# Performance work log

Hardware: AMD Instinct MI355X
Metric: run time of the kernel (lower is better)

Reference implementation:

```python
import jax, jax.numpy as jnp
import numpy as np

B, S, D = 2, 2048, 1024
H = 16
HD = D // H

def setup_inputs() -> dict:
    key = jax.random.key(0)
    ks = jax.random.split(key, 9)
    s = 1.0 / np.sqrt(D)
    return {
        "x": jax.random.normal(ks[0], (B, S, D), dtype=jnp.float32),
        "Wq": jax.random.normal(ks[1], (D, D), dtype=jnp.float32) * s,
        "bq": jnp.zeros((D,), dtype=jnp.float32),
        "Wk": jax.random.normal(ks[2], (D, D), dtype=jnp.float32) * s,
        "bk": jnp.zeros((D,), dtype=jnp.float32),
        "Wv": jax.random.normal(ks[3], (D, D), dtype=jnp.float32) * s,
        "bv": jnp.zeros((D,), dtype=jnp.float32),
        "Wo": jax.random.normal(ks[4], (D, D), dtype=jnp.float32) * s,
        "bo": jnp.zeros((D,), dtype=jnp.float32),
    }

def reference(x, Wq, bq, Wk, bk, Wv, bv, Wo, bo):
    b, s, d = x.shape
    # torch Linear: y = x @ W.T + b
    def proj(W, bias):
        y = jnp.einsum('bsd,ed->bse', x, W) + bias
        return y.reshape(b, s, H, HD).transpose(0, 2, 1, 3)  # [b,h,s,hd]
    Q = proj(Wq, bq)
    K = proj(Wk, bk)
    V = proj(Wv, bv)
    scale = 1.0 / jnp.sqrt(jnp.float32(HD))
    scores = jnp.einsum('bhqd,bhkd->bhqk', Q, K) * scale  # [b,h,s,s]
    attn = jax.nn.softmax(scores, axis=-1)
    out = jnp.einsum('bhqk,bhkd->bhqd', attn, V)  # [b,h,s,hd]
    out = out.transpose(0, 2, 1, 3).reshape(b, s, d)
    return jnp.einsum('bsd,ed->bse', out, Wo) + bo
```

## Files before the change

kernel.cpp:

```cpp
#include <hip/hip_runtime.h>
#include <stdint.h>


typedef __bf16 bf16x8 __attribute__((ext_vector_type(8)));
typedef float  f32x4  __attribute__((ext_vector_type(4)));
typedef unsigned short u16x8 __attribute__((ext_vector_type(8)));

#define LOG2E 1.44269504088896f
#define FIXED_MAX_BITS 14.4269504088896f

__device__ __forceinline__ unsigned short f2bf(float f) {
    union { float f; unsigned u; } v; v.f = f;
    unsigned r = v.u + 0x7FFFu + ((v.u >> 16) & 1u);
    return (unsigned short)(r >> 16);
}
__device__ __forceinline__ float bf2f(unsigned short u) {
    union { unsigned u; float f; } v; v.u = (unsigned)u << 16; return v.f;
}

__device__ __forceinline__ float exp2_fast(float x) {
#if __has_builtin(__builtin_amdgcn_exp2f)
    return __builtin_amdgcn_exp2f(x);
#else
    return __expf(x * 0.69314718056f);
#endif
}

__device__ __forceinline__ void glds16(const void* g, void* l) {
    __builtin_amdgcn_global_load_lds(
        (__attribute__((address_space(1))) void*)(g),
        (__attribute__((address_space(3))) void*)(l),
        16, 0, 0);
}

__global__ __launch_bounds__(256) void cvt_all(
    const float* __restrict__ x,  const float* __restrict__ Wq,
    const float* __restrict__ Wk, const float* __restrict__ Wv,
    const float* __restrict__ Wo,
    unsigned short* __restrict__ xb,  unsigned short* __restrict__ Wqb,
    unsigned short* __restrict__ Wkb, unsigned short* __restrict__ Wvb,
    unsigned short* __restrict__ Wob)
{
    const int stride = gridDim.x * blockDim.x;
    for (int i = blockIdx.x * blockDim.x + threadIdx.x; i < 2097152; i += stride) {
        const float* src; unsigned short* dst; int j;
        if (i < 1048576) { src = x; dst = xb; j = i; }
        else {
            int t = (i - 1048576) >> 18; j = (i - 1048576) & 262143;
            src = (t == 0) ? Wq : (t == 1) ? Wk : (t == 2) ? Wv : Wo;
            dst = (t == 0) ? Wqb : (t == 1) ? Wkb : (t == 2) ? Wvb : Wob;
        }
        float4 v = ((const float4*)src)[j];
        ushort4 o;
        o.x = f2bf(v.x); o.y = f2bf(v.y); o.z = f2bf(v.z); o.w = f2bf(v.w);
        ((ushort4*)dst)[j] = o;
    }
}

template <int MODE>
__global__ __launch_bounds__(256) void gemm_bt(
    const unsigned short* __restrict__ A,
    const unsigned short* __restrict__ W0,
    const unsigned short* __restrict__ W1,
    const unsigned short* __restrict__ W2,
    const float* __restrict__ b0,
    const float* __restrict__ b1,
    const float* __restrict__ b2,
    unsigned short* __restrict__ outQ,
    unsigned short* __restrict__ outK,
    unsigned short* __restrict__ outV,
    float* __restrict__ outF)
{
    constexpr int BM = (MODE == 0) ? 128 : 64;
    constexpr int FM = BM / 32;
    constexpr int RA = BM / 32;

    __shared__ __attribute__((aligned(16))) unsigned short As[BM * 64];
    __shared__ __attribute__((aligned(16))) unsigned short Bs[128 * 64];

    const int tid  = threadIdx.x;
    const int lane = tid & 63;
    const int wid  = tid >> 6;
    const int quad = lane >> 4;
    const int l16  = lane & 15;

    const int m0 = blockIdx.x * BM;

    const unsigned short* W;
    const float* bias;
    int proj, n0;
    if (MODE == 0) {
        proj = blockIdx.y >> 3;
        n0   = (blockIdx.y & 7) * 128;
        W    = (proj == 0) ? W0 : (proj == 1) ? W1 : W2;
        bias = (proj == 0) ? b0 : (proj == 1) ? b1 : b2;
    } else {
        proj = 0;
        n0   = blockIdx.y * 128;
        W    = W0;
        bias = b0;
    }

    const int wm = (wid >> 1) * (BM / 2);
    const int wn = (wid & 1) * 64;

    f32x4 acc[FM][4];
#pragma unroll
    for (int i = 0; i < FM; ++i)
#pragma unroll
        for (int j = 0; j < 4; ++j)
            acc[i][j] = (f32x4){0.f, 0.f, 0.f, 0.f};

    char* AsB  = (char*)As;
    char* BsB  = (char*)Bs;
    char* ldsA = AsB + wid * 1024;
    char* ldsB = BsB + wid * 1024;

    for (int k0 = 0; k0 < 1024; k0 += 64) {
#pragma unroll
        for (int q = 0; q < RA; ++q) {
            int i   = q * 256 + tid;
            int row = i >> 3;
            int sc  = (i & 7) ^ (row & 7);
            glds16(A + (size_t)(m0 + row) * 1024 + k0 + sc * 8, ldsA + q * 4096);
        }
#pragma unroll
        for (int q = 0; q < 4; ++q) {
            int i   = q * 256 + tid;
            int row = i >> 3;
            int sc  = (i & 7) ^ (row & 7);
            glds16(W + (size_t)(n0 + row) * 1024 + k0 + sc * 8, ldsB + q * 4096);
        }
        __syncthreads();

#pragma unroll
        for (int kh = 0; kh < 2; ++kh) {
            bf16x8 af[FM], bfr[4];
#pragma unroll
            for (int t = 0; t < FM; ++t) {
                int r = wm + t * 16 + l16;
                int c = (kh * 4 + quad) ^ (r & 7);
                af[t] = *(const bf16x8*)(AsB + r * 128 + c * 16);
            }
#pragma unroll
            for (int t = 0; t < 4; ++t) {
                int r = wn + t * 16 + l16;
                int c = (kh * 4 + quad) ^ (r & 7);
                bfr[t] = *(const bf16x8*)(BsB + r * 128 + c * 16);
            }
#pragma unroll
            for (int i = 0; i < FM; ++i)
#pragma unroll
                for (int j = 0; j < 4; ++j)
                    acc[i][j] = __builtin_amdgcn_mfma_f32_16x16x32_bf16(
                        af[i], bfr[j], acc[i][j], 0, 0, 0);
        }
        __syncthreads();
    }

#pragma unroll
    for (int i = 0; i < FM; ++i) {
        const int mrow0 = m0 + wm + i * 16 + quad * 4;
#pragma unroll
        for (int j = 0; j < 4; ++j) {
            const int n  = n0 + wn + j * 16 + l16;
            const float bb = bias[n];
            if (MODE == 1) {
#pragma unroll
                for (int r = 0; r < 4; ++r)
                    outF[(size_t)(mrow0 + r) * 1024 + n] = acc[i][j][r] + bb;
            } else {
                const int h = n >> 6, hd = n & 63;
                if (proj == 2) {
                    const int b = mrow0 >> 11, s = mrow0 & 2047;
                    ushort4 pk;
                    pk.x = f2bf(acc[i][j][0] + bb);
                    pk.y = f2bf(acc[i][j][1] + bb);
                    pk.z = f2bf(acc[i][j][2] + bb);
                    pk.w = f2bf(acc[i][j][3] + bb);
                    *(ushort4*)(outV + ((size_t)((b * 16 + h) * 64 + hd)) * 2048 + s) = pk;
                } else {
                    unsigned short* dst = (proj == 0) ? outQ : outK;
                    const float scl = (proj == 0) ? (0.125f * LOG2E) : 1.0f;
#pragma unroll
                    for (int r = 0; r < 4; ++r) {
                        const int m = mrow0 + r;
                        const int b = m >> 11, s = m & 2047;
                        dst[((size_t)((b * 16 + h) * 2048 + s)) * 64 + hd] =
                            f2bf((acc[i][j][r] + bb) * scl);
                    }
                }
            }
        }
    }
}

__global__ __launch_bounds__(256, 4) void attn_kernel(
    const unsigned short* __restrict__ Qb,
    const unsigned short* __restrict__ Kb,
    const unsigned short* __restrict__ Vtb,
    unsigned short* __restrict__ attnb)
{
    __shared__ __attribute__((aligned(16))) unsigned short Ks[128 * 64];
    __shared__ __attribute__((aligned(16))) unsigned short Vs[2 * 64 * 64];

    const int tid  = threadIdx.x;
    const int lane = tid & 63;
    const int wid  = tid >> 6;
    const int quad = lane >> 4;
    const int l16  = lane & 15;
    const int l7   = l16 & 7;

    const int q0   = blockIdx.x * 128 + wid * 32;
    const int hb   = blockIdx.y;
    const int bq   = hb >> 4, hh = hb & 15;

    const unsigned short* Qh  = Qb  + (size_t)hb * 2048 * 64;
    const unsigned short* Kh  = Kb  + (size_t)hb * 2048 * 64;
    const unsigned short* Vth = Vtb + (size_t)hb * 64 * 2048;

    bf16x8 qf[2][2];
#pragma unroll
    for (int qt = 0; qt < 2; ++qt) {
        const unsigned short* qp = Qh + (size_t)(q0 + qt * 16 + l16) * 64 + quad * 8;
        qf[qt][0] = *(const bf16x8*)(qp);
        qf[qt][1] = *(const bf16x8*)(qp + 32);
    }

    f32x4 o[4][2];
#pragma unroll
    for (int ht = 0; ht < 4; ++ht)
#pragma unroll
        for (int qt = 0; qt < 2; ++qt)
            o[ht][qt] = (f32x4){0.f, 0.f, 0.f, 0.f};
    float lsum[2] = {0.f, 0.f};

    char* KsB  = (char*)Ks;
    char* ldsK = KsB + wid * 1024;

    const int base_row = 8 * (l16 >> 2) + (l16 & 3);
    const int kp0 = ((quad) ^ l7) * 16;
    const int kp1 = ((4 + quad) ^ l7) * 16;
    const int vrow = l16 * 128;

    for (int kc = 0; kc < 2048; kc += 128) {
#pragma unroll
        for (int q = 0; q < 4; ++q) {
            int i   = q * 256 + tid;
            int row = i >> 3;
            int g   = (row & 3) | (((row >> 3) & 1) << 2);
            int ch  = (i & 7) ^ g;
            glds16(Kh + (size_t)(kc + row) * 64 + ch * 8, ldsK + q * 4096);
        }
#pragma unroll
        for (int sub = 0; sub < 2; ++sub)
#pragma unroll
            for (int q = 0; q < 2; ++q) {
                int i   = q * 256 + tid;
                int row = i >> 3;
                int ch  = (i & 7) ^ (row & 7);
                glds16(Vth + (size_t)row * 2048 + kc + sub * 64 + ch * 8,
                       (char*)Vs + sub * 8192 + wid * 1024 + q * 4096);
            }
        __syncthreads();

#pragma unroll
        for (int st32 = 0; st32 < 4; ++st32) {
            const char* krb = KsB + (st32 * 32 + base_row) * 128;
            bf16x8 kf00 = *(const bf16x8*)(krb + kp0);
            bf16x8 kf01 = *(const bf16x8*)(krb + kp1);
            bf16x8 kf10 = *(const bf16x8*)(krb + 512 + kp0);
            bf16x8 kf11 = *(const bf16x8*)(krb + 512 + kp1);

            const f32x4 mi = (f32x4){-FIXED_MAX_BITS, -FIXED_MAX_BITS,
                                     -FIXED_MAX_BITS, -FIXED_MAX_BITS};
            f32x4 s00 = mi, s01 = mi, s10 = mi, s11 = mi;
            s00 = __builtin_amdgcn_mfma_f32_16x16x32_bf16(kf00, qf[0][0], s00, 0, 0, 0);
            s00 = __builtin_amdgcn_mfma_f32_16x16x32_bf16(kf01, qf[0][1], s00, 0, 0, 0);
            s01 = __builtin_amdgcn_mfma_f32_16x16x32_bf16(kf10, qf[0][0], s01, 0, 0, 0);
            s01 = __builtin_amdgcn_mfma_f32_16x16x32_bf16(kf11, qf[0][1], s01, 0, 0, 0);
            s10 = __builtin_amdgcn_mfma_f32_16x16x32_bf16(kf00, qf[1][0], s10, 0, 0, 0);
            s10 = __builtin_amdgcn_mfma_f32_16x16x32_bf16(kf01, qf[1][1], s10, 0, 0, 0);
            s11 = __builtin_amdgcn_mfma_f32_16x16x32_bf16(kf10, qf[1][0], s11, 0, 0, 0);
            s11 = __builtin_amdgcn_mfma_f32_16x16x32_bf16(kf11, qf[1][1], s11, 0, 0, 0);

            bf16x8 p8[2];
#pragma unroll
            for (int qt = 0; qt < 2; ++qt) {
                const f32x4 sA = qt ? s10 : s00;
                const f32x4 sB = qt ? s11 : s01;
                float e0 = exp2_fast(sA[0]), e1 = exp2_fast(sA[1]);
                float e2 = exp2_fast(sA[2]), e3 = exp2_fast(sA[3]);
                float e4 = exp2_fast(sB[0]), e5 = exp2_fast(sB[1]);
                float e6 = exp2_fast(sB[2]), e7 = exp2_fast(sB[3]);
                lsum[qt] += ((e0 + e1) + (e2 + e3)) + ((e4 + e5) + (e6 + e7));
                bf16x8 p;
                p[0] = (__bf16)e0; p[1] = (__bf16)e1;
                p[2] = (__bf16)e2; p[3] = (__bf16)e3;
                p[4] = (__bf16)e4; p[5] = (__bf16)e5;
                p[6] = (__bf16)e6; p[7] = (__bf16)e7;
                p8[qt] = p;
            }

            const int voff = (st32 >> 1) * 8192 + vrow
                           + ((((st32 & 1) * 4 + quad) ^ l7) * 16);
#pragma unroll
            for (int ht = 0; ht < 4; ++ht) {
                const bf16x8 vf = *(const bf16x8*)((char*)Vs + voff + ht * 2048);
                o[ht][0] = __builtin_amdgcn_mfma_f32_16x16x32_bf16(vf, p8[0], o[ht][0], 0, 0, 0);
                o[ht][1] = __builtin_amdgcn_mfma_f32_16x16x32_bf16(vf, p8[1], o[ht][1], 0, 0, 0);
            }
        }
        __syncthreads();
    }

    float rl[2];
#pragma unroll
    for (int qt = 0; qt < 2; ++qt) {
        float s = lsum[qt];
        s += __shfl_xor(s, 16);
        s += __shfl_xor(s, 32);
        rl[qt] = 1.0f / s;
    }

#pragma unroll
    for (int qt = 0; qt < 2; ++qt) {
        const size_t row = (size_t)(bq * 2048 + q0 + qt * 16 + l16);
        const float r = rl[qt];
#pragma unroll
        for (int ht = 0; ht < 4; ++ht) {
            ushort4 pk;
            pk.x = f2bf(o[ht][qt][0] * r);
            pk.y = f2bf(o[ht][qt][1] * r);
            pk.z = f2bf(o[ht][qt][2] * r);
            pk.w = f2bf(o[ht][qt][3] * r);
            *(ushort4*)(attnb + row * 1024 + hh * 64 + ht * 16 + quad * 4) = pk;
        }
    }
}

extern "C" void kernel_launch(void* const* d_in, const int* in_sizes, int n_in,
                              void* d_out, int out_size, void* d_ws, size_t ws_size,
                              hipStream_t stream) {
    (void)in_sizes; (void)n_in; (void)out_size; (void)ws_size;

    const float* x  = (const float*)d_in[0];
    const float* Wq = (const float*)d_in[1];
    const float* bq = (const float*)d_in[2];
    const float* Wk = (const float*)d_in[3];
    const float* bk = (const float*)d_in[4];
    const float* Wv = (const float*)d_in[5];
    const float* bv = (const float*)d_in[6];
    const float* Wo = (const float*)d_in[7];
    const float* bo = (const float*)d_in[8];

    char* ws = (char*)d_ws;
    const size_t MB = 1024 * 1024;
    unsigned short* xb    = (unsigned short*)(ws + 0);
    unsigned short* Wqb   = (unsigned short*)(ws + 8  * MB);
    unsigned short* Wkb   = (unsigned short*)(ws + 10 * MB);
    unsigned short* Wvb   = (unsigned short*)(ws + 12 * MB);
    unsigned short* Wob   = (unsigned short*)(ws + 14 * MB);
    unsigned short* Qb    = (unsigned short*)(ws + 16 * MB);
    unsigned short* Kb    = (unsigned short*)(ws + 24 * MB);
    unsigned short* Vtb   = (unsigned short*)(ws + 32 * MB);
    unsigned short* attnb = (unsigned short*)(ws + 40 * MB);

    cvt_all<<<dim3(1024), dim3(256), 0, stream>>>(
        x, Wq, Wk, Wv, Wo, xb, Wqb, Wkb, Wvb, Wob);

    gemm_bt<0><<<dim3(32, 24), dim3(256), 0, stream>>>(
        xb, Wqb, Wkb, Wvb, bq, bk, bv, Qb, Kb, Vtb, nullptr);

    attn_kernel<<<dim3(16, 32), dim3(256), 0, stream>>>(Qb, Kb, Vtb, attnb);

    gemm_bt<1><<<dim3(64, 8), dim3(256), 0, stream>>>(
        attnb, Wob, nullptr, nullptr, bo, nullptr, nullptr,
        nullptr, nullptr, nullptr, (float*)d_out);
}
```

Measured before the change: 192.1 us.

## Double-buffer LDS tiles in GEMM and attention, remap attention blocks by head

Both the projection GEMM and the attention kernel now keep two LDS buffers. The next K-tile (or K/V chunk) is loaded asynchronously while the current one is being computed, which removes one barrier per iteration and overlaps global loads with MFMA work. The attention kernel also remaps its block index so that consecutive blocks cover eight heads within one query-tile group, aiming for better L2 reuse of K/V. The cost is that per-block LDS doubles, to about 64KB in attention, which may limit how many blocks fit on each CU below the launch-bound target.

```diff
diff --git a/kernel.cpp b/kernel.cpp
--- a/kernel.cpp
+++ b/kernel.cpp
@@ -4,7 +4,6 @@
 
 typedef __bf16 bf16x8 __attribute__((ext_vector_type(8)));
 typedef float  f32x4  __attribute__((ext_vector_type(4)));
-typedef unsigned short u16x8 __attribute__((ext_vector_type(8)));
 
 #define LOG2E 1.44269504088896f
 #define FIXED_MAX_BITS 14.4269504088896f
@@ -13,9 +12,6 @@
     union { float f; unsigned u; } v; v.f = f;
     unsigned r = v.u + 0x7FFFu + ((v.u >> 16) & 1u);
     return (unsigned short)(r >> 16);
-}
-__device__ __forceinline__ float bf2f(unsigned short u) {
-    union { unsigned u; float f; } v; v.u = (unsigned)u << 16; return v.f;
 }
 
 __device__ __forceinline__ float exp2_fast(float x) {
@@ -75,8 +71,8 @@
     constexpr int FM = BM / 32;
     constexpr int RA = BM / 32;
 
-    __shared__ __attribute__((aligned(16))) unsigned short As[BM * 64];
-    __shared__ __attribute__((aligned(16))) unsigned short Bs[128 * 64];
+    __shared__ __attribute__((aligned(16))) unsigned short As[2 * BM * 64];
+    __shared__ __attribute__((aligned(16))) unsigned short Bs[2 * 128 * 64];
 
     const int tid  = threadIdx.x;
     const int lane = tid & 63;
@@ -111,12 +107,12 @@
         for (int j = 0; j < 4; ++j)
             acc[i][j] = (f32x4){0.f, 0.f, 0.f, 0.f};
 
-    char* AsB  = (char*)As;
-    char* BsB  = (char*)Bs;
-    char* ldsA = AsB + wid * 1024;
-    char* ldsB = BsB + wid * 1024;
-
-    for (int k0 = 0; k0 < 1024; k0 += 64) {
+    char* AsB = (char*)As;
+    char* BsB = (char*)Bs;
+
+    auto stageAB = [&](int k0, int buf) {
+        char* ldsA = AsB + buf * (BM * 128) + wid * 1024;
+        char* ldsB = BsB + buf * 16384 + wid * 1024;
 #pragma unroll
         for (int q = 0; q < RA; ++q) {
             int i   = q * 256 + tid;
@@ -131,7 +127,17 @@
             int sc  = (i & 7) ^ (row & 7);
             glds16(W + (size_t)(n0 + row) * 1024 + k0 + sc * 8, ldsB + q * 4096);
         }
-        __syncthreads();
+    };
+
+    stageAB(0, 0);
+    __syncthreads();
+
+    for (int k0 = 0; k0 < 1024; k0 += 64) {
+        const int cur = (k0 >> 6) & 1;
+        if (k0 + 64 < 1024) stageAB(k0 + 64, cur ^ 1);
+
+        const char* AsC = AsB + cur * (BM * 128);
+        const char* BsC = BsB + cur * 16384;
 
 #pragma unroll
         for (int kh = 0; kh < 2; ++kh) {
@@ -140,13 +146,13 @@
             for (int t = 0; t < FM; ++t) {
                 int r = wm + t * 16 + l16;
                 int c = (kh * 4 + quad) ^ (r & 7);
-                af[t] = *(const bf16x8*)(AsB + r * 128 + c * 16);
+                af[t] = *(const bf16x8*)(AsC + r * 128 + c * 16);
             }
 #pragma unroll
             for (int t = 0; t < 4; ++t) {
                 int r = wn + t * 16 + l16;
                 int c = (kh * 4 + quad) ^ (r & 7);
-                bfr[t] = *(const bf16x8*)(BsB + r * 128 + c * 16);
+                bfr[t] = *(const bf16x8*)(BsC + r * 128 + c * 16);
             }
 #pragma unroll
             for (int i = 0; i < FM; ++i)
@@ -201,8 +207,8 @@
     const unsigned short* __restrict__ Vtb,
     unsigned short* __restrict__ attnb)
 {
-    __shared__ __attribute__((aligned(16))) unsigned short Ks[128 * 64];
-    __shared__ __attribute__((aligned(16))) unsigned short Vs[2 * 64 * 64];
+    __shared__ __attribute__((aligned(16))) unsigned short Ks[2 * 128 * 64];
+    __shared__ __attribute__((aligned(16))) unsigned short Vs[2 * 2 * 64 * 64];
 
     const int tid  = threadIdx.x;
     const int lane = tid & 63;
@@ -211,8 +217,13 @@
     const int l16  = lane & 15;
     const int l7   = l16 & 7;
 
-    const int q0   = blockIdx.x * 128 + wid * 32;
-    const int hb   = blockIdx.y;
+    const int bid  = blockIdx.x + (blockIdx.y << 4);
+    const int c8   = bid & 7;
+    const int t    = bid >> 3;
+    const int qt16 = t & 15;
+    const int hgrp = t >> 4;
+    const int hb   = c8 + (hgrp << 3);
+    const int q0   = qt16 * 128 + wid * 32;
     const int bq   = hb >> 4, hh = hb & 15;
 
     const unsigned short* Qh  = Qb  + (size_t)hb * 2048 * 64;
@@ -235,15 +246,11 @@
             o[ht][qt] = (f32x4){0.f, 0.f, 0.f, 0.f};
     float lsum[2] = {0.f, 0.f};
 
-    char* KsB  = (char*)Ks;
-    char* ldsK = KsB + wid * 1024;
-
-    const int base_row = 8 * (l16 >> 2) + (l16 & 3);
-    const int kp0 = ((quad) ^ l7) * 16;
-    const int kp1 = ((4 + quad) ^ l7) * 16;
-    const int vrow = l16 * 128;
-
-    for (int kc = 0; kc < 2048; kc += 128) {
+    char* KsB = (char*)Ks;
+    char* VsB = (char*)Vs;
+
+    auto stageKV = [&](int kc, int buf) {
+        char* ldsK = KsB + buf * 16384 + wid * 1024;
 #pragma unroll
         for (int q = 0; q < 4; ++q) {
             int i   = q * 256 + tid;
@@ -252,6 +259,7 @@
             int ch  = (i & 7) ^ g;
             glds16(Kh + (size_t)(kc + row) * 64 + ch * 8, ldsK + q * 4096);
         }
+        char* ldsV = VsB + buf * 16384;
 #pragma unroll
         for (int sub = 0; sub < 2; ++sub)
 #pragma unroll
@@ -260,13 +268,28 @@
                 int row = i >> 3;
                 int ch  = (i & 7) ^ (row & 7);
                 glds16(Vth + (size_t)row * 2048 + kc + sub * 64 + ch * 8,
-                       (char*)Vs + sub * 8192 + wid * 1024 + q * 4096);
-            }
-        __syncthreads();
+                       ldsV + sub * 8192 + wid * 1024 + q * 4096);
+            }
+    };
+
+    const int base_row = 8 * (l16 >> 2) + (l16 & 3);
+    const int kp0 = ((quad) ^ l7) * 16;
+    const int kp1 = ((4 + quad) ^ l7) * 16;
+    const int vrow = l16 * 128;
+
+    stageKV(0, 0);
+    __syncthreads();
+
+    for (int kc = 0; kc < 2048; kc += 128) {
+        const int cur = (kc >> 7) & 1;
+        if (kc + 128 < 2048) stageKV(kc + 128, cur ^ 1);
+
+        const char* KsC = KsB + cur * 16384;
+        const char* VsC = VsB + cur * 16384;
 
 #pragma unroll
         for (int st32 = 0; st32 < 4; ++st32) {
-            const char* krb = KsB + (st32 * 32 + base_row) * 128;
+            const char* krb = KsC + (st32 * 32 + base_row) * 128;
             bf16x8 kf00 = *(const bf16x8*)(krb + kp0);
             bf16x8 kf01 = *(const bf16x8*)(krb + kp1);
             bf16x8 kf10 = *(const bf16x8*)(krb + 512 + kp0);
@@ -306,7 +329,7 @@
                            + ((((st32 & 1) * 4 + quad) ^ l7) * 16);
 #pragma unroll
             for (int ht = 0; ht < 4; ++ht) {
-                const bf16x8 vf = *(const bf16x8*)((char*)Vs + voff + ht * 2048);
+                const bf16x8 vf = *(const bf16x8*)(VsC + voff + ht * 2048);
                 o[ht][0] = __builtin_amdgcn_mfma_f32_16x16x32_bf16(vf, p8[0], o[ht][0], 0, 0, 0);
                 o[ht][1] = __builtin_amdgcn_mfma_f32_16x16x32_bf16(vf, p8[1], o[ht][1], 0, 0, 0);
             }
```

Result: no change. 191.6 us (-0.3%).
